# Kernel optimization log

Measured on AMD Instinct MI355X. Metric: run time of the kernel, lower is better.

Reference implementation:

```python
import jax, jax.numpy as jnp
import numpy as np

CLAMP_MAX = float(np.log(100.0))  # temperature clamp from MoELayer


def setup_inputs() -> dict:
    key = jax.random.key(0)
    ks = jax.random.split(key, 4)
    N, D, H, E = 524288, 128, 512, 8
    x = jax.random.normal(ks[0], (N, D), dtype=jnp.float32)
    # per-expert MLP params, stacked along expert axis; scaled like torch Linear init
    W1 = jax.random.normal(ks[1], (E, D, H), dtype=jnp.float32) / np.sqrt(D)
    b1 = jnp.zeros((E, H), dtype=jnp.float32)
    W2 = jax.random.normal(ks[2], (E, H, D), dtype=jnp.float32) / np.sqrt(H)
    b2 = jnp.zeros((E, D), dtype=jnp.float32)
    temperature = jnp.full((1,), np.log(2.0), dtype=jnp.float32)  # init from MoELayer
    return {"x": x, "W1": W1, "b1": b1, "W2": W2, "b2": b2,
            "temperature": temperature}


def reference(x, W1, b1, W2, b2, temperature):
    # Pretraining proportional router: tokens split into E contiguous equal
    # chunks (route_prob == 1), so dispatch/combine is a reshape.
    E = W1.shape[0]
    N, D = x.shape
    xe = x.reshape(E, N // E, D)                      # [E, n, D] dispatched tokens
    h = jax.nn.relu(jnp.einsum('end,edh->enh', xe, W1) + b1[:, None, :])
    y = jnp.einsum('enh,ehd->end', h, W2) + b2[:, None, :]
    logit_scale = jnp.exp(jnp.minimum(temperature, CLAMP_MAX))  # scalar [1]
    out = y.reshape(N, D) * logit_scale
    return out
```

## Files before the change

kernel.cpp:

```cpp
#include <hip/hip_runtime.h>


#define CLAMP_MAXV 4.605170185988091f

typedef __attribute__((ext_vector_type(8))) short s16x8;
typedef __attribute__((ext_vector_type(4))) float f32x4;
typedef __attribute__((ext_vector_type(4))) unsigned short u16x4;
typedef __attribute__((ext_vector_type(8))) unsigned short u16x8;

static __device__ __forceinline__ unsigned short f2bf(float f) {
  union { float f; unsigned int u; } v; v.f = f;
  unsigned int r = v.u + 0x7FFFu + ((v.u >> 16) & 1u);
  return (unsigned short)(r >> 16);
}

static __device__ __forceinline__ void gll16(const void* src, void* dst) {
  __builtin_amdgcn_global_load_lds((const __attribute__((address_space(1))) void*)src,
                                   (__attribute__((address_space(3))) void*)dst, 16, 0, 0);
}

#define LBAR() do { \
  asm volatile("s_waitcnt lgkmcnt(0)" ::: "memory"); \
  __builtin_amdgcn_s_barrier(); \
  __builtin_amdgcn_sched_barrier(0); \
} while (0)

__global__ void conv_w(const float* __restrict__ W1, const float* __restrict__ W2,
                       unsigned short* __restrict__ w1t, unsigned short* __restrict__ w2t) {
  int idx = blockIdx.x * 256 + threadIdx.x;
  if (idx < 65536) {
    int h  = idx & 511;
    int d0 = ((idx >> 9) & 15) << 3;
    int e  = idx >> 13;
    const float* src = W1 + ((size_t)e << 16);
    u16x8 v;
#pragma unroll
    for (int j = 0; j < 8; ++j) v[j] = f2bf(src[(size_t)(d0 + j) * 512 + h]);
    *(u16x8*)(w1t + ((((size_t)e << 9) + h) << 7) + d0) = v;
  } else {
    int i2 = idx - 65536;
    int d  = i2 & 127;
    int h0 = ((i2 >> 7) & 63) << 3;
    int e  = i2 >> 13;
    const float* src = W2 + ((size_t)e << 16);
    u16x8 v;
#pragma unroll
    for (int j = 0; j < 8; ++j) v[j] = f2bf(src[(size_t)(h0 + j) * 128 + d]);
    *(u16x8*)(w2t + ((((size_t)e << 7) + d) << 9) + h0) = v;
  }
}

__global__ __launch_bounds__(1024, 4) void moe_fused(
    const float* __restrict__ x,
    const float* __restrict__ b1,
    const float* __restrict__ b2,
    const float* __restrict__ temp,
    const unsigned short* __restrict__ w1t,
    const unsigned short* __restrict__ w2t,
    float* __restrict__ out)
{
  __shared__ __align__(16) char smem[149504];
  char* const w1s  = smem;
  char* const hsb0 = smem + 131072;
  char* const hsb1 = smem + 139264;
  char* const xs   = smem + 131072;
  float* const b1s = (float*)(smem + 147456);

  const int tid  = threadIdx.x;
  const int lane = tid & 63;
  const int wid  = tid >> 6;
  const int l15  = lane & 15;
  const int lg   = lane >> 4;
  const int blk  = blockIdx.x;
  const int e    = blk >> 6;
  const size_t tok0 = (size_t)blk << 10;

  const unsigned short* w1g = w1t + ((size_t)e << 16);
  const unsigned short* w2g = w2t + ((size_t)e << 16);
  const float* xblk = x + (tok0 << 7);
  float* const oblk = out + (tok0 << 7);

#pragma unroll
  for (int k = 0; k < 8; ++k) {
    int s = tid + (k << 10);
    int h = s >> 4, sr = s & 15;
    gll16(w1g + ((size_t)h << 7) + ((sr ^ (h & 7)) << 3), w1s + (s << 4));
  }

  if (tid < 512) b1s[tid] = b1[(e << 9) + tid];

  f32x4 xv[2];
  xv[0] = *(const f32x4*)(xblk + (tid << 3));
  xv[1] = *(const f32x4*)(xblk + (tid << 3) + 4);

  __syncthreads();

  const int xtok = tid >> 4;
  const unsigned xaddr = (unsigned)((xtok << 8) + ((tid & 15) << 4)) ^ (unsigned)((xtok & 7) << 4);

  if (wid < 8) {
    const int hr  = wid & 3;
    const int tq0 = (wid >> 2) << 5;
    const unsigned hl2 = (unsigned)(((hr << 4) + (lg << 2)) << 1);

#pragma unroll 1
    for (int t = 0; t < 16; ++t) {
      u16x8 p;
#pragma unroll
      for (int i = 0; i < 8; ++i) p[i] = f2bf(xv[i >> 2][i & 3]);
      *(u16x8*)(xs + xaddr) = p;
      LBAR();

      s16x8 xb[2][4];
#pragma unroll
      for (int j = 0; j < 2; ++j) {
        int tk = tq0 + (j << 4) + l15;
#pragma unroll
        for (int ks = 0; ks < 4; ++ks) {
          unsigned koff = (unsigned)((ks << 6) + (lg << 4));
          xb[j][ks] = *(const s16x8*)(xs + (((unsigned)(tk << 8) + koff) ^ (unsigned)((tk & 7) << 4)));
        }
      }
      LBAR();

#pragma unroll
      for (int c = 0; c <= 8; ++c) {
        if (c < 8) {
          const int hrow = (c << 6) + (hr << 4) + l15;
          const unsigned hswz = (unsigned)((hrow & 7) << 4);
          s16x8 a[4];
#pragma unroll
          for (int ks = 0; ks < 4; ++ks) {
            unsigned koff = (unsigned)((ks << 6) + (lg << 4));
            a[ks] = *(const s16x8*)(w1s + (((unsigned)(hrow << 8) + koff) ^ hswz));
          }
          f32x4 bias = *(const f32x4*)(b1s + (c << 6) + (hr << 4) + (lg << 2));
          f32x4 acc1[2];
          acc1[0] = (f32x4){0.f, 0.f, 0.f, 0.f};
          acc1[1] = (f32x4){0.f, 0.f, 0.f, 0.f};
#pragma unroll
          for (int j = 0; j < 2; ++j)
#pragma unroll
            for (int ks = 0; ks < 4; ++ks)
              acc1[j] = __builtin_amdgcn_mfma_f32_16x16x32_bf16(a[ks], xb[j][ks], acc1[j], 0, 0, 0);

          char* const hw = (c & 1) ? hsb1 : hsb0;
#pragma unroll
          for (int j = 0; j < 2; ++j) {
            int tk = tq0 + (j << 4) + l15;
            u16x4 q;
#pragma unroll
            for (int r = 0; r < 4; ++r)
              q[r] = f2bf(fmaxf(acc1[j][r] + bias[r], 0.f));
            *(u16x4*)(hw + (((unsigned)(tk << 7) + hl2) ^ (unsigned)((tk & 7) << 4))) = q;
          }
        }
        if (c == 4 && t < 15) {
          const float* xn = xblk + (((size_t)t + 1) << 13);
          xv[0] = *(const f32x4*)(xn + (tid << 3));
          xv[1] = *(const f32x4*)(xn + (tid << 3) + 4);
        }
        LBAR();
      }
    }
  } else {
    const int cw = wid - 8;
    const int dlane = (cw << 4) + l15;

    s16x8 w2f[8][2];
#pragma unroll
    for (int c = 0; c < 8; ++c)
#pragma unroll
      for (int ks = 0; ks < 2; ++ks)
        w2f[c][ks] = *(const s16x8*)(w2g + ((size_t)dlane << 9) + (c << 6) + (ks << 5) + (lg << 3));

    const float b2v   = b2[(e << 7) + dlane];
    const float scale = expf(fminf(temp[0], CLAMP_MAXV));

#pragma unroll 1
    for (int t = 0; t < 16; ++t) {
      u16x8 p;
#pragma unroll
      for (int i = 0; i < 8; ++i) p[i] = f2bf(xv[i >> 2][i & 3]);
      *(u16x8*)(xs + xaddr) = p;
      LBAR();
      LBAR();

      f32x4 acc2[4];
#pragma unroll
      for (int i = 0; i < 4; ++i) acc2[i] = (f32x4){0.f, 0.f, 0.f, 0.f};

#pragma unroll
      for (int c = 0; c <= 8; ++c) {
        if (c >= 1) {
          const int cc = c - 1;
          char* const hrd = (cc & 1) ? hsb1 : hsb0;
#pragma unroll
          for (int i = 0; i < 4; ++i) {
            int tk = (i << 4) + l15;
            unsigned tswz = (unsigned)((tk & 7) << 4);
#pragma unroll
            for (int ks = 0; ks < 2; ++ks) {
              unsigned koff = (unsigned)((ks << 6) + (lg << 4));
              s16x8 ha = *(const s16x8*)(hrd + (((unsigned)(tk << 7) + koff) ^ tswz));
              acc2[i] = __builtin_amdgcn_mfma_f32_16x16x32_bf16(ha, w2f[cc][ks], acc2[i], 0, 0, 0);
            }
          }
        }
        if (c == 4 && t < 15) {
          const float* xn = xblk + (((size_t)t + 1) << 13);
          xv[0] = *(const f32x4*)(xn + (tid << 3));
          xv[1] = *(const f32x4*)(xn + (tid << 3) + 4);
        }
        LBAR();
      }

      float* og = oblk + ((size_t)t << 13);
#pragma unroll
      for (int i = 0; i < 4; ++i) {
#pragma unroll
        for (int r = 0; r < 4; ++r) {
          int tk = (i << 4) + (lg << 2) + r;
          og[((size_t)tk << 7) + dlane] = (acc2[i][r] + b2v) * scale;
        }
      }
    }
  }
}

__global__ void moe_naive(const float* __restrict__ x, const float* __restrict__ W1,
                          const float* __restrict__ b1, const float* __restrict__ W2,
                          const float* __restrict__ b2, const float* __restrict__ temp,
                          float* __restrict__ out) {
  __shared__ float xr[128];
  __shared__ float hrow[512];
  int t = blockIdx.x;
  int e = t >> 16;
  int tx = threadIdx.x;
  xr[tx] = x[((size_t)t << 7) + tx];
  __syncthreads();
  const float* w1e = W1 + ((size_t)e << 16);
  for (int h = tx; h < 512; h += 128) {
    float s = b1[(e << 9) + h];
    for (int d = 0; d < 128; ++d) s += xr[d] * w1e[(size_t)d * 512 + h];
    hrow[h] = fmaxf(s, 0.f);
  }
  __syncthreads();
  const float* w2e = W2 + ((size_t)e << 16);
  float s = b2[(e << 7) + tx];
  for (int h = 0; h < 512; ++h) s += hrow[h] * w2e[(size_t)h * 128 + tx];
  out[((size_t)t << 7) + tx] = s * expf(fminf(temp[0], CLAMP_MAXV));
}

extern "C" void kernel_launch(void* const* d_in, const int* in_sizes, int n_in,
                              void* d_out, int out_size, void* d_ws, size_t ws_size,
                              hipStream_t stream) {
  const float* x    = (const float*)d_in[0];
  const float* W1   = (const float*)d_in[1];
  const float* b1   = (const float*)d_in[2];
  const float* W2   = (const float*)d_in[3];
  const float* b2   = (const float*)d_in[4];
  const float* temp = (const float*)d_in[5];
  float* out = (float*)d_out;

  const size_t WS_NEEDED = 2u * 524288u * sizeof(unsigned short);
  if (ws_size >= WS_NEEDED) {
    unsigned short* w1t = (unsigned short*)d_ws;
    unsigned short* w2t = w1t + 524288;
    conv_w<<<512, 256, 0, stream>>>(W1, W2, w1t, w2t);
    moe_fused<<<512, 1024, 0, stream>>>(x, b1, b2, temp, w1t, w2t, out);
  } else {
    moe_naive<<<524288, 128, 0, stream>>>(x, W1, b1, W2, b2, temp, out);
  }
}
```

Baseline: 178.3 us.

## Stream W1 MFMA fragments from global in fragment-packed layout instead of LDS

W1 is now repacked by the conversion kernel into an MFMA-fragment-ordered layout, so each lane reads its A fragments with one contiguous 16-byte global load per k-step. The 128KB W1 copy in LDS is removed, and each chunk's fragments are prefetched one step ahead into double-buffered registers. This frees LDS, which could allow more blocks to be resident, and drops the up-front W1 staging. The cost is re-reading W1 from global/L2 on every token tile and extra register pressure.

```diff
diff --git a/kernel.cpp b/kernel.cpp
--- a/kernel.cpp
+++ b/kernel.cpp
@@ -12,11 +12,6 @@
   union { float f; unsigned int u; } v; v.f = f;
   unsigned int r = v.u + 0x7FFFu + ((v.u >> 16) & 1u);
   return (unsigned short)(r >> 16);
-}
-
-static __device__ __forceinline__ void gll16(const void* src, void* dst) {
-  __builtin_amdgcn_global_load_lds((const __attribute__((address_space(1))) void*)src,
-                                   (__attribute__((address_space(3))) void*)dst, 16, 0, 0);
 }
 
 #define LBAR() do { \
@@ -26,7 +21,7 @@
 } while (0)
 
 __global__ void conv_w(const float* __restrict__ W1, const float* __restrict__ W2,
-                       unsigned short* __restrict__ w1t, unsigned short* __restrict__ w2t) {
+                       unsigned short* __restrict__ w1p, unsigned short* __restrict__ w2t) {
   int idx = blockIdx.x * 256 + threadIdx.x;
   if (idx < 65536) {
     int h  = idx & 511;
@@ -36,7 +31,10 @@
     u16x8 v;
 #pragma unroll
     for (int j = 0; j < 8; ++j) v[j] = f2bf(src[(size_t)(d0 + j) * 512 + h]);
-    *(u16x8*)(w1t + ((((size_t)e << 9) + h) << 7) + d0) = v;
+    int c = h >> 6, hr = (h >> 4) & 3, l15 = h & 15;
+    int ks = d0 >> 5, lg = (d0 >> 3) & 3;
+    size_t idx8 = ((size_t)(((c << 2) + hr) << 2 | ks) << 6) + (l15 << 2) + lg;
+    *(u16x8*)(w1p + ((size_t)e << 16) + (idx8 << 3)) = v;
   } else {
     int i2 = idx - 65536;
     int d  = i2 & 127;
@@ -55,16 +53,15 @@
     const float* __restrict__ b1,
     const float* __restrict__ b2,
     const float* __restrict__ temp,
-    const unsigned short* __restrict__ w1t,
+    const unsigned short* __restrict__ w1p,
     const unsigned short* __restrict__ w2t,
     float* __restrict__ out)
 {
-  __shared__ __align__(16) char smem[149504];
-  char* const w1s  = smem;
-  char* const hsb0 = smem + 131072;
-  char* const hsb1 = smem + 139264;
-  char* const xs   = smem + 131072;
-  float* const b1s = (float*)(smem + 147456);
+  __shared__ __align__(16) char smem[18432];
+  char* const hsb0 = smem;
+  char* const hsb1 = smem + 8192;
+  char* const xs   = smem;
+  float* const b1s = (float*)(smem + 16384);
 
   const int tid  = threadIdx.x;
   const int lane = tid & 63;
@@ -75,17 +72,10 @@
   const int e    = blk >> 6;
   const size_t tok0 = (size_t)blk << 10;
 
-  const unsigned short* w1g = w1t + ((size_t)e << 16);
+  const unsigned short* w1g = w1p + ((size_t)e << 16);
   const unsigned short* w2g = w2t + ((size_t)e << 16);
   const float* xblk = x + (tok0 << 7);
   float* const oblk = out + (tok0 << 7);
-
-#pragma unroll
-  for (int k = 0; k < 8; ++k) {
-    int s = tid + (k << 10);
-    int h = s >> 4, sr = s & 15;
-    gll16(w1g + ((size_t)h << 7) + ((sr ^ (h & 7)) << 3), w1s + (s << 4));
-  }
 
   if (tid < 512) b1s[tid] = b1[(e << 9) + tid];
 
@@ -102,6 +92,12 @@
     const int hr  = wid & 3;
     const int tq0 = (wid >> 2) << 5;
     const unsigned hl2 = (unsigned)(((hr << 4) + (lg << 2)) << 1);
+    const unsigned lofs = (unsigned)((l15 << 5) + (lg << 3));
+
+    s16x8 afr[2][4];
+#pragma unroll
+    for (int ks = 0; ks < 4; ++ks)
+      afr[0][ks] = *(const s16x8*)(w1g + ((unsigned)hr << 11) + (ks << 9) + lofs);
 
 #pragma unroll 1
     for (int t = 0; t < 16; ++t) {
@@ -126,14 +122,12 @@
 #pragma unroll
       for (int c = 0; c <= 8; ++c) {
         if (c < 8) {
-          const int hrow = (c << 6) + (hr << 4) + l15;
-          const unsigned hswz = (unsigned)((hrow & 7) << 4);
-          s16x8 a[4];
-#pragma unroll
-          for (int ks = 0; ks < 4; ++ks) {
-            unsigned koff = (unsigned)((ks << 6) + (lg << 4));
-            a[ks] = *(const s16x8*)(w1s + (((unsigned)(hrow << 8) + koff) ^ hswz));
-          }
+          const int nc = (c + 1) & 7;
+          const unsigned arow = (unsigned)((nc << 2) + hr);
+#pragma unroll
+          for (int ks = 0; ks < 4; ++ks)
+            afr[(c + 1) & 1][ks] = *(const s16x8*)(w1g + (arow << 11) + (ks << 9) + lofs);
+
           f32x4 bias = *(const f32x4*)(b1s + (c << 6) + (hr << 4) + (lg << 2));
           f32x4 acc1[2];
           acc1[0] = (f32x4){0.f, 0.f, 0.f, 0.f};
@@ -142,7 +136,7 @@
           for (int j = 0; j < 2; ++j)
 #pragma unroll
             for (int ks = 0; ks < 4; ++ks)
-              acc1[j] = __builtin_amdgcn_mfma_f32_16x16x32_bf16(a[ks], xb[j][ks], acc1[j], 0, 0, 0);
+              acc1[j] = __builtin_amdgcn_mfma_f32_16x16x32_bf16(afr[c & 1][ks], xb[j][ks], acc1[j], 0, 0, 0);
 
           char* const hw = (c & 1) ? hsb1 : hsb0;
 #pragma unroll
@@ -265,10 +259,10 @@
 
   const size_t WS_NEEDED = 2u * 524288u * sizeof(unsigned short);
   if (ws_size >= WS_NEEDED) {
-    unsigned short* w1t = (unsigned short*)d_ws;
-    unsigned short* w2t = w1t + 524288;
-    conv_w<<<512, 256, 0, stream>>>(W1, W2, w1t, w2t);
-    moe_fused<<<512, 1024, 0, stream>>>(x, b1, b2, temp, w1t, w2t, out);
+    unsigned short* w1p = (unsigned short*)d_ws;
+    unsigned short* w2t = w1p + 524288;
+    conv_w<<<512, 256, 0, stream>>>(W1, W2, w1p, w2t);
+    moe_fused<<<512, 1024, 0, stream>>>(x, b1, b2, temp, w1p, w2t, out);
   } else {
     moe_naive<<<524288, 128, 0, stream>>>(x, W1, b1, W2, b2, temp, out);
   }
```

Result: slower. 203.6 us (+14.2%).

## Hold first W1 chunks in registers and give x its own LDS buffer

Applied to the files above, without the earlier changes.

The first two 64-row W1 chunks now live in producer-wave registers, and only the remaining 384 rows are staged in LDS. This frees space so the x staging buffer no longer aliases the h buffers, which lets one barrier per token tile be dropped in both producer and consumer waves. It trades extra VGPR pressure in the producer waves for less LDS traffic and fewer synchronisations. Dropping the barrier adds a risk of a race between the next tile's x write and the current tile's x reads.

```diff
diff --git a/kernel.cpp b/kernel.cpp
--- a/kernel.cpp
+++ b/kernel.cpp
@@ -59,12 +59,12 @@
     const unsigned short* __restrict__ w2t,
     float* __restrict__ out)
 {
-  __shared__ __align__(16) char smem[149504];
+  __shared__ __align__(16) char smem[133120];
   char* const w1s  = smem;
-  char* const hsb0 = smem + 131072;
-  char* const hsb1 = smem + 139264;
-  char* const xs   = smem + 131072;
-  float* const b1s = (float*)(smem + 147456);
+  char* const hsb0 = smem + 98304;
+  char* const hsb1 = smem + 106496;
+  char* const xs   = smem + 114688;
+  float* const b1s = (float*)(smem + 131072);
 
   const int tid  = threadIdx.x;
   const int lane = tid & 63;
@@ -81,10 +81,10 @@
   float* const oblk = out + (tok0 << 7);
 
 #pragma unroll
-  for (int k = 0; k < 8; ++k) {
+  for (int k = 0; k < 6; ++k) {
     int s = tid + (k << 10);
-    int h = s >> 4, sr = s & 15;
-    gll16(w1g + ((size_t)h << 7) + ((sr ^ (h & 7)) << 3), w1s + (s << 4));
+    int hl = s >> 4, sr = s & 15;
+    gll16(w1g + ((size_t)(hl + 128) << 7) + ((sr ^ (hl & 7)) << 3), w1s + (s << 4));
   }
 
   if (tid < 512) b1s[tid] = b1[(e << 9) + tid];
@@ -92,8 +92,6 @@
   f32x4 xv[2];
   xv[0] = *(const f32x4*)(xblk + (tid << 3));
   xv[1] = *(const f32x4*)(xblk + (tid << 3) + 4);
-
-  __syncthreads();
 
   const int xtok = tid >> 4;
   const unsigned xaddr = (unsigned)((xtok << 8) + ((tid & 15) << 4)) ^ (unsigned)((xtok & 7) << 4);
@@ -103,6 +101,17 @@
     const int tq0 = (wid >> 2) << 5;
     const unsigned hl2 = (unsigned)(((hr << 4) + (lg << 2)) << 1);
 
+    s16x8 w1r[2][4];
+#pragma unroll
+    for (int c = 0; c < 2; ++c) {
+      const int hrow = (c << 6) + (hr << 4) + l15;
+#pragma unroll
+      for (int ks = 0; ks < 4; ++ks)
+        w1r[c][ks] = *(const s16x8*)(w1g + ((size_t)hrow << 7) + (ks << 5) + (lg << 3));
+    }
+
+    __syncthreads();
+
 #pragma unroll 1
     for (int t = 0; t < 16; ++t) {
       u16x8 p;
@@ -121,38 +130,45 @@
           xb[j][ks] = *(const s16x8*)(xs + (((unsigned)(tk << 8) + koff) ^ (unsigned)((tk & 7) << 4)));
         }
       }
-      LBAR();
 
 #pragma unroll
       for (int c = 0; c <= 8; ++c) {
         if (c < 8) {
-          const int hrow = (c << 6) + (hr << 4) + l15;
-          const unsigned hswz = (unsigned)((hrow & 7) << 4);
-          s16x8 a[4];
-#pragma unroll
-          for (int ks = 0; ks < 4; ++ks) {
-            unsigned koff = (unsigned)((ks << 6) + (lg << 4));
-            a[ks] = *(const s16x8*)(w1s + (((unsigned)(hrow << 8) + koff) ^ hswz));
-          }
           f32x4 bias = *(const f32x4*)(b1s + (c << 6) + (hr << 4) + (lg << 2));
           f32x4 acc1[2];
           acc1[0] = (f32x4){0.f, 0.f, 0.f, 0.f};
           acc1[1] = (f32x4){0.f, 0.f, 0.f, 0.f};
-#pragma unroll
-          for (int j = 0; j < 2; ++j)
-#pragma unroll
-            for (int ks = 0; ks < 4; ++ks)
-              acc1[j] = __builtin_amdgcn_mfma_f32_16x16x32_bf16(a[ks], xb[j][ks], acc1[j], 0, 0, 0);
+          if (c < 2) {
+#pragma unroll
+            for (int j = 0; j < 2; ++j)
+#pragma unroll
+              for (int ks = 0; ks < 4; ++ks)
+                acc1[j] = __builtin_amdgcn_mfma_f32_16x16x32_bf16(w1r[c][ks], xb[j][ks], acc1[j], 0, 0, 0);
+          } else {
+            const int hrow = (c << 6) + (hr << 4) + l15;
+            const unsigned hswz = (unsigned)((hrow & 7) << 4);
+            s16x8 a[4];
+#pragma unroll
+            for (int ks = 0; ks < 4; ++ks) {
+              unsigned koff = (unsigned)((ks << 6) + (lg << 4));
+              a[ks] = *(const s16x8*)(w1s + (((unsigned)((hrow - 128) << 8) + koff) ^ hswz));
+            }
+#pragma unroll
+            for (int j = 0; j < 2; ++j)
+#pragma unroll
+              for (int ks = 0; ks < 4; ++ks)
+                acc1[j] = __builtin_amdgcn_mfma_f32_16x16x32_bf16(a[ks], xb[j][ks], acc1[j], 0, 0, 0);
+          }
 
           char* const hw = (c & 1) ? hsb1 : hsb0;
 #pragma unroll
           for (int j = 0; j < 2; ++j) {
             int tk = tq0 + (j << 4) + l15;
-            u16x4 q;
+            u16x4 qv;
 #pragma unroll
             for (int r = 0; r < 4; ++r)
-              q[r] = f2bf(fmaxf(acc1[j][r] + bias[r], 0.f));
-            *(u16x4*)(hw + (((unsigned)(tk << 7) + hl2) ^ (unsigned)((tk & 7) << 4))) = q;
+              qv[r] = f2bf(fmaxf(acc1[j][r] + bias[r], 0.f));
+            *(u16x4*)(hw + (((unsigned)(tk << 7) + hl2) ^ (unsigned)((tk & 7) << 4))) = qv;
           }
         }
         if (c == 4 && t < 15) {
@@ -177,13 +193,14 @@
     const float b2v   = b2[(e << 7) + dlane];
     const float scale = expf(fminf(temp[0], CLAMP_MAXV));
 
+    __syncthreads();
+
 #pragma unroll 1
     for (int t = 0; t < 16; ++t) {
       u16x8 p;
 #pragma unroll
       for (int i = 0; i < 8; ++i) p[i] = f2bf(xv[i >> 2][i & 3]);
       *(u16x8*)(xs + xaddr) = p;
-      LBAR();
       LBAR();
 
       f32x4 acc2[4];
@@ -196,14 +213,14 @@
           const int cc = c - 1;
           char* const hrd = (cc & 1) ? hsb1 : hsb0;
 #pragma unroll
-          for (int i = 0; i < 4; ++i) {
-            int tk = (i << 4) + l15;
+          for (int ii = 0; ii < 4; ++ii) {
+            int tk = (ii << 4) + l15;
             unsigned tswz = (unsigned)((tk & 7) << 4);
 #pragma unroll
             for (int ks = 0; ks < 2; ++ks) {
               unsigned koff = (unsigned)((ks << 6) + (lg << 4));
               s16x8 ha = *(const s16x8*)(hrd + (((unsigned)(tk << 7) + koff) ^ tswz));
-              acc2[i] = __builtin_amdgcn_mfma_f32_16x16x32_bf16(ha, w2f[cc][ks], acc2[i], 0, 0, 0);
+              acc2[ii] = __builtin_amdgcn_mfma_f32_16x16x32_bf16(ha, w2f[cc][ks], acc2[ii], 0, 0, 0);
             }
           }
         }
```

After: 178.6 us. About the same (+0.2%).
